# Kernel optimization log

Hardware: AMD Instinct MI355X
Metric: run time of the kernel (lower is better)

## Reference

```python
import jax, jax.numpy as jnp
import numpy as np

COMMITMENT_COST = 0.25
NUM_CODES = 4096
EMBED_DIM = 64


def setup_inputs() -> dict:
    key = jax.random.key(0)
    k1, k2 = jax.random.split(key)
    z_e = jax.random.normal(k1, (65536, EMBED_DIM), dtype=jnp.float32)
    embeddings = jax.random.normal(k2, (NUM_CODES, EMBED_DIM), dtype=jnp.float32)
    return {"z_e": z_e, "embeddings": embeddings}


def reference(z_e, embeddings):
    # Squared Euclidean distances; argmin is identical to torch.cdist argmin.
    # d2[n,k] = |z_e[n]|^2 - 2 z_e[n].e[k] + |e[k]|^2
    z_sq = jnp.sum(z_e * z_e, axis=-1, keepdims=True)            # [N,1]
    e_sq = jnp.sum(embeddings * embeddings, axis=-1)              # [K]
    d2 = z_sq - 2.0 * jnp.einsum('nd,kd->nk', z_e, embeddings) + e_sq  # [N,K]
    indices = jnp.argmin(d2, axis=-1)                             # [N] int
    z_q = embeddings[indices]                                     # [N,D] gather

    # commitment loss = mse(stop_grad(z_q), z_e)
    commitment_loss = COMMITMENT_COST * jnp.mean(
        (jax.lax.stop_gradient(z_q) - z_e) ** 2)

    # straight-through estimator
    z_q_st = z_e + jax.lax.stop_gradient(z_q - z_e)

    # code usage stats: one-hot mean == normalized histogram (scatter-add)
    n = z_e.shape[0]
    counts = jnp.zeros((NUM_CODES,), dtype=jnp.float32).at[indices].add(1.0)
    avg_probs = counts / n
    perplexity = jnp.exp(-jnp.sum(avg_probs * jnp.log(avg_probs + 1e-10)))
    n_active = jnp.sum(avg_probs > 0.001)

    return z_q_st, indices, commitment_loss, perplexity, n_active
```

## Files before the change

kernel.cpp:

```cpp
#include <hip/hip_runtime.h>
#include <math.h>

#define D 64
#define K 4096
#define MARGIN 0.08f
#define KSPLIT 4
#define CPH (K / 16 / KSPLIT)
#define TS 8
#define NT (CPH / TS)
#define TROWS 32

typedef float f32x4 __attribute__((ext_vector_type(4)));
typedef _Float16 f16x8 __attribute__((ext_vector_type(8)));

#define GLOAD_LDS(g, l)                                              \
  __builtin_amdgcn_global_load_lds(                                  \
      (const __attribute__((address_space(1))) void*)(g),            \
      (__attribute__((address_space(3))) void*)(l), 16, 0, 0)

__global__ __launch_bounds__(256) void esplit_kernel(const float* __restrict__ emb,
                                                     short* __restrict__ e_h,
                                                     float* __restrict__ e_sq,
                                                     int* __restrict__ counts,
                                                     int* __restrict__ ctrl) {
  int i = blockIdx.x * 256 + threadIdx.x;
  {
    int lane = i & 63;
    int t = (i >> 6) & 1;
    int c = i >> 7;
    int quad = lane >> 4, col = lane & 15;
    const float* src = emb + (size_t)(c * 16 + col) * D + t * 32 + quad * 8;
    f32x4 u0 = *(const f32x4*)src;
    f32x4 u1 = *(const f32x4*)(src + 4);
    f16x8 h;
#pragma unroll
    for (int j = 0; j < 8; ++j) {
      float x = (j < 4) ? u0[j] : u1[j - 4];
      h[j] = (_Float16)x;
    }
    *(f16x8*)(e_h + (size_t)i * 8) = h;
  }
  if (i < 128) ctrl[i] = 0;
  if (i < K) {
    counts[i] = 0;
    const float* e = emb + (size_t)i * D;
    float s = 0.f;
#pragma unroll
    for (int d = 0; d < D; ++d) s = fmaf(e[d], e[d], s);
    e_sq[i] = s;
  }
}

#define MFMA16(A, B, C) __builtin_amdgcn_mfma_f32_16x16x32_f16(A, B, C, 0, 0, 0)

__global__ __launch_bounds__(256, 2) void dist_kernel(const float* __restrict__ z_e,
                                                      const short* __restrict__ e_h,
                                                      const float* __restrict__ esq,
                                                      float* __restrict__ pbest,
                                                      float* __restrict__ psec,
                                                      int* __restrict__ pidx) {
  const int tid = threadIdx.x;
  const int wv = tid >> 6;
  const int lane = tid & 63;
  const int quad = lane >> 4, col = lane & 15;
  const int rowbase = blockIdx.x * 128 + wv * 32;
  const int half = blockIdx.y;
  const int c0 = half * CPH;

  __shared__ __align__(16) short sbuf[2 * TS * 1024];

  f16x8 a[2][2];
#pragma unroll
  for (int s = 0; s < 2; ++s) {
#pragma unroll
    for (int t = 0; t < 2; ++t) {
      const float* zr = z_e + (size_t)(rowbase + s * 16 + col) * D + t * 32 + quad * 8;
      f32x4 u0 = *(const f32x4*)zr;
      f32x4 u1 = *(const f32x4*)(zr + 4);
#pragma unroll
      for (int j = 0; j < 8; ++j) {
        float x = (j < 4) ? u0[j] : u1[j - 4];
        a[s][t][j] = (_Float16)x;
      }
    }
  }

  float best[8], second[8];
  int bidx[8];
#pragma unroll
  for (int i = 0; i < 8; ++i) {
    best[i] = -__builtin_inff();
    second[i] = -__builtin_inff();
    bidx[i] = 0;
  }

  const short* gB = e_h + (size_t)c0 * 1024;
  const float* pE = esq + c0 * 16 + col;

  {
    const short* src = gB + (size_t)wv * 2048 + (size_t)lane * 8;
    short* dst = sbuf + wv * 2048;
#pragma unroll
    for (int s = 0; s < 4; ++s) GLOAD_LDS(src + s * 512, dst + s * 512);
  }

  unsigned rbase = 0;
  for (int t = 0; t < NT; ++t) {
    __syncthreads();

    if (t + 1 < NT) {
      const short* src = gB + (size_t)(t + 1) * (TS * 1024) + wv * 2048 + lane * 8;
      short* dst = sbuf + (rbase ^ (TS * 1024)) + wv * 2048;
#pragma unroll
      for (int s = 0; s < 4; ++s) GLOAD_LDS(src + s * 512, dst + s * 512);
    }

    float eqt[TS];
#pragma unroll
    for (int j = 0; j < TS; ++j) eqt[j] = pE[(t * TS + j) * 16];

    const short* sB = sbuf + rbase;
#pragma unroll
    for (int j = 0; j < TS; ++j) {
      f16x8 b0 = *(const f16x8*)(sB + j * 1024 + lane * 8);
      f16x8 b1 = *(const f16x8*)(sB + j * 1024 + 512 + lane * 8);

      const float seed = -0.5f * eqt[j];
      f32x4 acc0 = {seed, seed, seed, seed};
      f32x4 acc1 = {seed, seed, seed, seed};
      acc0 = MFMA16(a[0][0], b0, acc0);
      acc1 = MFMA16(a[1][0], b0, acc1);
      acc0 = MFMA16(a[0][1], b1, acc0);
      acc1 = MFMA16(a[1][1], b1, acc1);

      const int cc = t * TS + j;
#pragma unroll
      for (int r = 0; r < 4; ++r) {
        float a0 = acc0[r];
        float ob = best[r];
        best[r] = fmaxf(ob, a0);
        second[r] = __builtin_amdgcn_fmed3f(ob, a0, second[r]);
        bidx[r] = (a0 > ob) ? cc : bidx[r];
      }
#pragma unroll
      for (int r = 0; r < 4; ++r) {
        float a1 = acc1[r];
        float ob = best[4 + r];
        best[4 + r] = fmaxf(ob, a1);
        second[4 + r] = __builtin_amdgcn_fmed3f(ob, a1, second[4 + r]);
        bidx[4 + r] = (a1 > ob) ? cc : bidx[4 + r];
      }
    }
    rbase ^= TS * 1024;
  }

#pragma unroll
  for (int i = 0; i < 8; ++i) {
    float b = -2.f * best[i];
    float s2 = -2.f * second[i];
    int ix = (c0 + bidx[i]) * 16 + col;
#pragma unroll
    for (int off = 1; off < 16; off <<= 1) {
      float ob = __shfl_xor(b, off);
      float os = __shfl_xor(s2, off);
      int oi = __shfl_xor(ix, off);
      float ns = fminf(fminf(s2, os), fmaxf(b, ob));
      if (ob < b || (ob == b && oi < ix)) ix = oi;
      b = fminf(b, ob);
      s2 = ns;
    }
    if (col == 0) {
      int row = rowbase + (i >> 2) * 16 + quad * 4 + (i & 3);
      size_t o = (size_t)half * 65536 + row;
      pbest[o] = b;
      psec[o] = s2;
      pidx[o] = ix;
    }
  }
}

__global__ __launch_bounds__(256) void tail_kernel(const float* __restrict__ z_e,
                                                   const float* __restrict__ emb,
                                                   const float* __restrict__ esq,
                                                   const float* __restrict__ pbest,
                                                   const float* __restrict__ psec,
                                                   const int* __restrict__ pidx,
                                                   float* __restrict__ out_zq,
                                                   float* __restrict__ out_idx,
                                                   int* __restrict__ counts,
                                                   int* __restrict__ ctrl,
                                                   float* __restrict__ out_scalars,
                                                   int N) {
  const int tid = threadIdx.x;
  const int wave = tid >> 6;
  const int lane = tid & 63;
  const int base = blockIdx.x * TROWS;
  int* done = ctrl;
  float* loss_slots = (float*)(ctrl + 8);

  __shared__ int wl[TROWS];
  __shared__ int bidx_s[TROWS];
  __shared__ int wn;
  __shared__ int lastflag;
  __shared__ float zs[4][D];
  __shared__ float se[4];
  __shared__ int sa[4];

  if (tid == 0) wn = 0;
  __syncthreads();

  if (tid < TROWS) {
    int row = base + tid;
    float b = pbest[row];
    float s2 = psec[row];
    int ix = pidx[row];
#pragma unroll
    for (int h = 1; h < KSPLIT; ++h) {
      size_t o = (size_t)h * 65536 + row;
      float bh = pbest[o];
      float sh = psec[o];
      int ih = pidx[o];
      s2 = fminf(fminf(s2, sh), fmaxf(b, bh));
      if (bh < b) ix = ih;
      b = fminf(b, bh);
    }
    bidx_s[tid] = ix;
    if (s2 - b < MARGIN) {
      int slot = atomicAdd(&wn, 1);
      wl[slot] = row;
    }
  }
  __syncthreads();

  const int n = wn;
  for (int j = wave; j < n; j += 4) {
    const int row = wl[j];
    if (lane < 16) ((f32x4*)zs[wave])[lane] = *((const f32x4*)(z_e + (size_t)row * D) + lane);

    float pb[KSPLIT], ps[KSPLIT];
    int pi[KSPLIT];
    float B = __builtin_inff();
#pragma unroll
    for (int h = 0; h < KSPLIT; ++h) {
      size_t o = (size_t)h * 65536 + row;
      pb[h] = pbest[o];
      ps[h] = psec[o];
      pi[h] = pidx[o];
      B = fminf(B, pb[h]);
    }
    const float lim = B + MARGIN;

    float bv = __builtin_inff();
    int bi = 0;
#pragma unroll
    for (int h = 0; h < KSPLIT; ++h) {
      if (ps[h] < lim) {
        float hb = __builtin_inff();
        int hx = 0;
        for (int t = 0; t < 16; ++t) {
          int c = h * 1024 + t * 64 + lane;
          const f32x4* er = (const f32x4*)(emb + (size_t)c * D);
          f32x4 a = {0.f, 0.f, 0.f, 0.f};
#pragma unroll
          for (int i = 0; i < 16; ++i)
            a = __builtin_elementwise_fma(er[i], ((const f32x4*)zs[wave])[i], a);
          float dot = (a[0] + a[1]) + (a[2] + a[3]);
          float q = fmaf(-2.f, dot, esq[c]);
          if (q < hb) { hb = q; hx = c; }
        }
#pragma unroll
        for (int off = 32; off > 0; off >>= 1) {
          float ov = __shfl_down(hb, off);
          int oi = __shfl_down(hx, off);
          if (ov < hb || (ov == hb && oi < hx)) { hb = ov; hx = oi; }
        }
        hb = __shfl(hb, 0);
        hx = __shfl(hx, 0);
        if (hb < bv || (hb == bv && hx < bi)) { bv = hb; bi = hx; }
      } else if (pb[h] < lim) {
        int c = pi[h];
        float p = emb[(size_t)c * D + lane] * zs[wave][lane];
#pragma unroll
        for (int off = 1; off < 64; off <<= 1) p += __shfl_xor(p, off);
        float q = fmaf(-2.f, p, esq[c]);
        if (q < bv || (q == bv && c < bi)) { bv = q; bi = c; }
      }
    }
    if (lane == 0) bidx_s[row - base] = bi;
  }
  __syncthreads();

  float lloss = 0.f;
  for (int r = wave; r < TROWS; r += 8) {
    const int r1 = r + 4;
    const int i0 = bidx_s[r];
    const int i1 = bidx_s[r1];
    const size_t row0 = base + r, row1 = base + r1;
    float ze0 = z_e[row0 * D + lane];
    float ze1 = z_e[row1 * D + lane];
    float zq0 = emb[(size_t)i0 * D + lane];
    float zq1 = emb[(size_t)i1 * D + lane];
    out_zq[row0 * D + lane] = ze0 + (zq0 - ze0);
    out_zq[row1 * D + lane] = ze1 + (zq1 - ze1);
    float d0 = zq0 - ze0, d1 = zq1 - ze1;
    lloss = fmaf(d0, d0, lloss);
    lloss = fmaf(d1, d1, lloss);
    if (lane == 0) {
      out_idx[row0] = (float)i0;
      out_idx[row1] = (float)i1;
      atomicAdd(&counts[i0], 1);
      atomicAdd(&counts[i1], 1);
    }
  }
#pragma unroll
  for (int off = 32; off > 0; off >>= 1) lloss += __shfl_down(lloss, off);
  if (lane == 0) atomicAdd(&loss_slots[blockIdx.x & 63], lloss);

  __syncthreads();
  if (tid == 0) {
    __threadfence();
    lastflag = (atomicAdd(done, 1) == (int)gridDim.x - 1);
  }
  __syncthreads();
  if (!lastflag) return;

  float ent = 0.f;
  int act = 0;
  const float invN = 1.0f / (float)N;
  for (int k = tid; k < K; k += 256) {
    float p = (float)atomicAdd(&counts[k], 0) * invN;
    ent += p * logf(p + 1e-10f);
    act += (p > 0.001f) ? 1 : 0;
  }
#pragma unroll
  for (int off = 32; off > 0; off >>= 1) {
    ent += __shfl_down(ent, off);
    act += __shfl_down(act, off);
  }
  if (lane == 0) { se[wave] = ent; sa[wave] = act; }

  float L = 0.f;
  if (wave == 0) {
    L = atomicAdd(&loss_slots[lane], 0.f);
#pragma unroll
    for (int off = 32; off > 0; off >>= 1) L += __shfl_down(L, off);
  }
  __syncthreads();
  if (tid == 0) {
    float E = se[0] + se[1] + se[2] + se[3];
    int A = sa[0] + sa[1] + sa[2] + sa[3];
    out_scalars[0] = 0.25f * L / ((float)N * (float)D);
    out_scalars[1] = expf(-E);
    out_scalars[2] = (float)A;
  }
}

extern "C" void kernel_launch(void* const* d_in, const int* in_sizes, int n_in,
                              void* d_out, int out_size, void* d_ws, size_t ws_size,
                              hipStream_t stream) {
  const float* z_e = (const float*)d_in[0];
  const float* emb = (const float*)d_in[1];
  const int N = in_sizes[0] / D;

  float* out = (float*)d_out;
  float* out_zq = out;
  float* out_idx = out + (size_t)N * D;
  float* out_scalars = out + (size_t)N * (D + 1);

  char* ws = (char*)d_ws;
  size_t o = 0;
  int* counts = (int*)(ws + o);      o += 16384;
  int* ctrl = (int*)(ws + o);        o += 512;
  float* esq = (float*)(ws + o);     o += 16384;
  short* e_h = (short*)(ws + o);     o += (size_t)K * D * 2;
  o += 8192;
  float* pbest = (float*)(ws + o);   o += (size_t)KSPLIT * N * 4;
  float* psec = (float*)(ws + o);    o += (size_t)KSPLIT * N * 4;
  int* pidx = (int*)(ws + o);        o += (size_t)KSPLIT * N * 4;

  esplit_kernel<<<(K / 16) * 2 * 64 / 256, 256, 0, stream>>>(emb, e_h, esq,
                                                             counts, ctrl);
  dist_kernel<<<dim3(N / 128, KSPLIT), 256, 0, stream>>>(z_e, e_h, esq,
                                                         pbest, psec, pidx);
  tail_kernel<<<N / TROWS, 256, 0, stream>>>(z_e, emb, esq, pbest, psec, pidx,
                                             out_zq, out_idx, counts, ctrl,
                                             out_scalars, N);
}
```

Measured before the change: 246.3 us.

## Replace last-block atomic reduction with separate stats kernel and larger tail tiles

The tail kernel no longer counts finished blocks atomically and no longer runs the entropy/loss reduction in the last block. Each block now writes its partial loss to a slot, and a new single-block 1024-thread kernel reduces losses and histogram counts. Rows per tail block grow from 32 to 128, giving fewer blocks and fewer partials. This removes the global atomics and fence but adds a kernel launch.

```diff
diff --git a/kernel.cpp b/kernel.cpp
--- a/kernel.cpp
+++ b/kernel.cpp
@@ -8,7 +8,7 @@
 #define CPH (K / 16 / KSPLIT)
 #define TS 8
 #define NT (CPH / TS)
-#define TROWS 32
+#define TROWS 128
 
 typedef float f32x4 __attribute__((ext_vector_type(4)));
 typedef _Float16 f16x8 __attribute__((ext_vector_type(8)));
@@ -21,8 +21,7 @@
 __global__ __launch_bounds__(256) void esplit_kernel(const float* __restrict__ emb,
                                                      short* __restrict__ e_h,
                                                      float* __restrict__ e_sq,
-                                                     int* __restrict__ counts,
-                                                     int* __restrict__ ctrl) {
+                                                     int* __restrict__ counts) {
   int i = blockIdx.x * 256 + threadIdx.x;
   {
     int lane = i & 63;
@@ -40,7 +39,6 @@
     }
     *(f16x8*)(e_h + (size_t)i * 8) = h;
   }
-  if (i < 128) ctrl[i] = 0;
   if (i < K) {
     counts[i] = 0;
     const float* e = emb + (size_t)i * D;
@@ -188,23 +186,17 @@
                                                    float* __restrict__ out_zq,
                                                    float* __restrict__ out_idx,
                                                    int* __restrict__ counts,
-                                                   int* __restrict__ ctrl,
-                                                   float* __restrict__ out_scalars,
-                                                   int N) {
+                                                   float* __restrict__ block_loss) {
   const int tid = threadIdx.x;
   const int wave = tid >> 6;
   const int lane = tid & 63;
   const int base = blockIdx.x * TROWS;
-  int* done = ctrl;
-  float* loss_slots = (float*)(ctrl + 8);
 
   __shared__ int wl[TROWS];
   __shared__ int bidx_s[TROWS];
   __shared__ int wn;
-  __shared__ int lastflag;
   __shared__ float zs[4][D];
-  __shared__ float se[4];
-  __shared__ int sa[4];
+  __shared__ float ls[4];
 
   if (tid == 0) wn = 0;
   __syncthreads();
@@ -314,41 +306,48 @@
   }
 #pragma unroll
   for (int off = 32; off > 0; off >>= 1) lloss += __shfl_down(lloss, off);
-  if (lane == 0) atomicAdd(&loss_slots[blockIdx.x & 63], lloss);
-
-  __syncthreads();
-  if (tid == 0) {
-    __threadfence();
-    lastflag = (atomicAdd(done, 1) == (int)gridDim.x - 1);
-  }
-  __syncthreads();
-  if (!lastflag) return;
+  if (lane == 0) ls[wave] = lloss;
+  __syncthreads();
+  if (tid == 0) block_loss[blockIdx.x] = ls[0] + ls[1] + ls[2] + ls[3];
+}
+
+__global__ __launch_bounds__(1024) void stats_kernel(const float* __restrict__ block_loss,
+                                                     int nblocks,
+                                                     const int* __restrict__ counts,
+                                                     float* __restrict__ out_scalars,
+                                                     int N) {
+  const int tid = threadIdx.x;
+  const int wave = tid >> 6;
+  const int lane = tid & 63;
+
+  float lsum = 0.f;
+  for (int i = tid; i < nblocks; i += 1024) lsum += block_loss[i];
 
   float ent = 0.f;
   int act = 0;
   const float invN = 1.0f / (float)N;
-  for (int k = tid; k < K; k += 256) {
-    float p = (float)atomicAdd(&counts[k], 0) * invN;
+  for (int k = tid; k < K; k += 1024) {
+    float p = (float)counts[k] * invN;
     ent += p * logf(p + 1e-10f);
     act += (p > 0.001f) ? 1 : 0;
   }
+
 #pragma unroll
   for (int off = 32; off > 0; off >>= 1) {
+    lsum += __shfl_down(lsum, off);
     ent += __shfl_down(ent, off);
     act += __shfl_down(act, off);
   }
-  if (lane == 0) { se[wave] = ent; sa[wave] = act; }
-
-  float L = 0.f;
-  if (wave == 0) {
-    L = atomicAdd(&loss_slots[lane], 0.f);
-#pragma unroll
-    for (int off = 32; off > 0; off >>= 1) L += __shfl_down(L, off);
-  }
+
+  __shared__ float sl[16], se[16];
+  __shared__ int sa[16];
+  if (lane == 0) { sl[wave] = lsum; se[wave] = ent; sa[wave] = act; }
   __syncthreads();
   if (tid == 0) {
-    float E = se[0] + se[1] + se[2] + se[3];
-    int A = sa[0] + sa[1] + sa[2] + sa[3];
+    float L = 0.f, E = 0.f;
+    int A = 0;
+#pragma unroll
+    for (int w = 0; w < 16; ++w) { L += sl[w]; E += se[w]; A += sa[w]; }
     out_scalars[0] = 0.25f * L / ((float)N * (float)D);
     out_scalars[1] = expf(-E);
     out_scalars[2] = (float)A;
@@ -370,7 +369,7 @@
   char* ws = (char*)d_ws;
   size_t o = 0;
   int* counts = (int*)(ws + o);      o += 16384;
-  int* ctrl = (int*)(ws + o);        o += 512;
+  float* block_loss = (float*)(ws + o); o += 4096;
   float* esq = (float*)(ws + o);     o += 16384;
   short* e_h = (short*)(ws + o);     o += (size_t)K * D * 2;
   o += 8192;
@@ -378,11 +377,11 @@
   float* psec = (float*)(ws + o);    o += (size_t)KSPLIT * N * 4;
   int* pidx = (int*)(ws + o);        o += (size_t)KSPLIT * N * 4;
 
-  esplit_kernel<<<(K / 16) * 2 * 64 / 256, 256, 0, stream>>>(emb, e_h, esq,
-                                                             counts, ctrl);
+  esplit_kernel<<<(K / 16) * 2 * 64 / 256, 256, 0, stream>>>(emb, e_h, esq, counts);
   dist_kernel<<<dim3(N / 128, KSPLIT), 256, 0, stream>>>(z_e, e_h, esq,
                                                          pbest, psec, pidx);
   tail_kernel<<<N / TROWS, 256, 0, stream>>>(z_e, emb, esq, pbest, psec, pidx,
-                                             out_zq, out_idx, counts, ctrl,
-                                             out_scalars, N);
-}
+                                             out_zq, out_idx, counts, block_loss);
+  stats_kernel<<<1, 1024, 0, stream>>>(block_loss, N / TROWS, counts,
+                                       out_scalars, N);
+}
```

After: 206.8 us. 1.19x faster.
